# Kernel optimization log

Measured on AMD Instinct MI355X. Metric: run time of the kernel, lower is better.

## Reference

```python
import jax, jax.numpy as jnp
import numpy as np

SIZE = (2, 2)


def setup_inputs() -> dict:
    key = jax.random.key(0)
    k1, k2 = jax.random.split(key)
    B, H, W, C = 32, 64, 64, 128
    out_flat = (H * SIZE[0]) * (W * SIZE[1]) * C  # 2,097,152
    updates = jax.random.normal(k1, (B, H, W, C), dtype=jnp.float32)
    mask = jax.random.randint(k2, (B, H, W, C), 0, out_flat, dtype=jnp.int32)
    return {"updates": updates, "mask": mask}


def reference(updates, mask):
    B, H, W, C = updates.shape
    outH, outW = H * SIZE[0], W * SIZE[1]
    flat = outH * outW * C
    # batch index broadcast to match mask, then flat scatter (tf.scatter_nd sums duplicates)
    b = jnp.broadcast_to(jnp.arange(B, dtype=jnp.int32)[:, None, None, None], mask.shape)
    ret = jnp.zeros((B, flat), dtype=updates.dtype)
    ret = ret.at[b.reshape(-1), mask.reshape(-1)].add(updates.reshape(-1))
    return ret.reshape(B, outH, outW, C)
```

## Files before the change

kernel.cpp:

```cpp
#include <hip/hip_runtime.h>


typedef float f32x4 __attribute__((ext_vector_type(4)));
typedef int i32x4 __attribute__((ext_vector_type(4)));
typedef unsigned u32x4 __attribute__((ext_vector_type(4)));

constexpr int B = 32;
constexpr int IN_PER_B = 1 << 19;
constexpr int OUT_PER_B = 1 << 21;
constexpr int N = B * IN_PER_B;
constexpr int OUT_N = B * OUT_PER_B;

constexpr int BKT_BITS = 13;
constexpr int BKT_SIZE = 1 << BKT_BITS;
constexpr int NBKT = B * (OUT_PER_B >> BKT_BITS);
constexpr int CAP = 3072;
constexpr int CHUNK = 4096;
constexpr int P1_THREADS = 512;
constexpr int P2_THREADS = 512;
constexpr int P1_BLOCKS = N / CHUNK;
constexpr unsigned DUMP_IDX = (unsigned)NBKT * (unsigned)CAP;
constexpr size_t BINS_BYTES = ((size_t)NBKT * CAP + 16) * 4ull;
constexpr size_t CNT_BYTES = (size_t)NBKT * 4ull;
constexpr size_t WS_NEEDED = BINS_BYTES + CNT_BYTES;

__device__ __forceinline__ unsigned pack_val19(float v) {
  unsigned bits = __float_as_uint(v);
  return (bits + 0x1000u) >> 13;
}
__device__ __forceinline__ float unpack_val19(unsigned p) {
  return __uint_as_float(p << 13);
}

__global__ __launch_bounds__(P1_THREADS) void p1_bin(const i32x4* __restrict__ msk,
                                                     const f32x4* __restrict__ upd,
                                                     unsigned* __restrict__ bins,
                                                     int* __restrict__ cnt) {
  __shared__ int hist[256];
  __shared__ int wsum[4];
  __shared__ unsigned adjg[256];
  __shared__ unsigned lsthr[256];
  __shared__ uint2 sdata[CHUNK];

  const int t = threadIdx.x;
  const int blk = blockIdx.x;
  const int b = blk >> 7;
  const long c4 = (long)blk * (CHUNK / 4);

  if (t < 256) hist[t] = 0;

  i32x4 m[2];
  f32x4 u[2];
#pragma unroll
  for (int k = 0; k < 2; k++) {
    m[k] = __builtin_nontemporal_load(&msk[c4 + k * P1_THREADS + t]);
    u[k] = __builtin_nontemporal_load(&upd[c4 + k * P1_THREADS + t]);
  }
  __syncthreads();

  int rank[8];
#pragma unroll
  for (int k = 0; k < 2; k++) {
#pragma unroll
    for (int c = 0; c < 4; c++)
      rank[k * 4 + c] = atomicAdd(&hist[m[k][c] >> BKT_BITS], 1);
  }
  __syncthreads();

  int h = 0, v = 0;
  if (t < 256) {
    h = hist[t];
    v = h;
#pragma unroll
    for (int off = 1; off < 64; off <<= 1) {
      int pv = __shfl_up(v, off);
      if ((t & 63) >= off) v += pv;
    }
    if ((t & 63) == 63) wsum[t >> 6] = v;
  }
  __syncthreads();
  if (t < 256) {
    const int w = t >> 6;
    int pre = 0;
    if (w > 0) pre += wsum[0];
    if (w > 1) pre += wsum[1];
    if (w > 2) pre += wsum[2];
    const int ls = pre + v - h;
    const int gb = (b << 8) + t;
    const int cbase = (h > 0) ? atomicAdd(&cnt[gb], h) : 0;
    adjg[t] = (unsigned)gb * (unsigned)CAP + (unsigned)(cbase - ls);
    int thr = CAP - cbase;
    thr = thr < 0 ? 0 : (thr > 0xFFFF ? 0xFFFF : thr);
    lsthr[t] = (unsigned)ls | ((unsigned)thr << 16);
  }
  __syncthreads();

#pragma unroll
  for (int k = 0; k < 2; k++) {
#pragma unroll
    for (int c = 0; c < 4; c++) {
      const int idx = m[k][c];
      const int bkt = idx >> BKT_BITS;
      const unsigned lt = lsthr[bkt];
      const int r = rank[k * 4 + c];
      const int pos = (int)(lt & 0xFFFFu) + r;
      unsigned g = adjg[bkt] + (unsigned)pos;
      if ((unsigned)r >= (lt >> 16)) g = DUMP_IDX;
      const unsigned pair =
          ((unsigned)(idx & (BKT_SIZE - 1)) << 19) | pack_val19(u[k][c]);
      sdata[pos] = make_uint2(pair, g);
    }
  }
  __syncthreads();

  const uint4* s4 = (const uint4*)sdata;
#pragma unroll
  for (int k = 0; k < CHUNK / 2 / P1_THREADS; k++) {
    uint4 e = s4[k * P1_THREADS + t];
    bins[e.y] = e.x;
    bins[e.w] = e.z;
  }
}

__global__ __launch_bounds__(P2_THREADS) void p2_acc(const unsigned* __restrict__ bins,
                                                     const int* __restrict__ cnt,
                                                     f32x4* __restrict__ out) {
  __shared__ float acc[BKT_SIZE];
  const int t = threadIdx.x;
  const int gb = blockIdx.x;

  int count = cnt[gb];
  if (count > CAP) count = CAP;
  const long base = (long)gb * CAP;
  const u32x4* b4 = (const u32x4*)(bins + base);
  const int nv = count >> 2;

  u32x4 v0 = (u32x4){0, 0, 0, 0}, v1 = v0;
  const bool h0 = t < nv, h1 = t + P2_THREADS < nv;
  if (h0) v0 = __builtin_nontemporal_load(&b4[t]);
  if (h1) v1 = __builtin_nontemporal_load(&b4[t + P2_THREADS]);
  const int rem = count - (nv << 2);
  unsigned tv = 0;
  const bool ht = t < rem;
  if (ht) tv = bins[base + (nv << 2) + t];

  f32x4* a4 = (f32x4*)acc;
#pragma unroll
  for (int k = 0; k < BKT_SIZE / 4 / P2_THREADS; k++)
    a4[k * P2_THREADS + t] = (f32x4){0.f, 0.f, 0.f, 0.f};
  __syncthreads();

  if (h0) {
    atomicAdd(&acc[v0.x >> 19], unpack_val19(v0.x));
    atomicAdd(&acc[v0.y >> 19], unpack_val19(v0.y));
    atomicAdd(&acc[v0.z >> 19], unpack_val19(v0.z));
    atomicAdd(&acc[v0.w >> 19], unpack_val19(v0.w));
  }
  if (h1) {
    atomicAdd(&acc[v1.x >> 19], unpack_val19(v1.x));
    atomicAdd(&acc[v1.y >> 19], unpack_val19(v1.y));
    atomicAdd(&acc[v1.z >> 19], unpack_val19(v1.z));
    atomicAdd(&acc[v1.w >> 19], unpack_val19(v1.w));
  }
  if (ht) atomicAdd(&acc[tv >> 19], unpack_val19(tv));
  __syncthreads();

  const long ob4 = (long)gb * (BKT_SIZE / 4);
#pragma unroll
  for (int k = 0; k < BKT_SIZE / 4 / P2_THREADS; k++) {
    f32x4 o = a4[k * P2_THREADS + t];
    __builtin_nontemporal_store(o, &out[ob4 + k * P2_THREADS + t]);
  }
}

__global__ __launch_bounds__(256) void zero_kernel(float4* __restrict__ out) {
  int i = blockIdx.x * 256 + threadIdx.x;
  out[i] = make_float4(0.f, 0.f, 0.f, 0.f);
}

__global__ __launch_bounds__(256) void scatter_atomic(const float4* __restrict__ upd,
                                                      const int4* __restrict__ msk,
                                                      float* __restrict__ out) {
  int i = blockIdx.x * 256 + threadIdx.x;
  int4 m = msk[i];
  float4 u = upd[i];
  int b = i >> 17;
  float* outb = out + (long)b * OUT_PER_B;
  unsafeAtomicAdd(outb + m.x, u.x);
  unsafeAtomicAdd(outb + m.y, u.y);
  unsafeAtomicAdd(outb + m.z, u.z);
  unsafeAtomicAdd(outb + m.w, u.w);
}

extern "C" void kernel_launch(void* const* d_in, const int* in_sizes, int n_in,
                              void* d_out, int out_size, void* d_ws, size_t ws_size,
                              hipStream_t stream) {
  if (ws_size >= WS_NEEDED) {
    unsigned* bins = (unsigned*)d_ws;
    int* cnt = (int*)((char*)d_ws + BINS_BYTES);
    (void)hipMemsetAsync(cnt, 0, CNT_BYTES, stream);
    p1_bin<<<P1_BLOCKS, P1_THREADS, 0, stream>>>((const i32x4*)d_in[1],
                                                 (const f32x4*)d_in[0], bins, cnt);
    p2_acc<<<NBKT, P2_THREADS, 0, stream>>>(bins, cnt, (f32x4*)d_out);
  } else {
    zero_kernel<<<OUT_N / 4 / 256, 256, 0, stream>>>((float4*)d_out);
    scatter_atomic<<<N / 4 / 256, 256, 0, stream>>>((const float4*)d_in[0],
                                                    (const int4*)d_in[1],
                                                    (float*)d_out);
  }
}
```

Baseline: 421.0 us.

## Pad bucket segments to multiples of four and emit 16-byte vector bin stores

Each bucket's per-chunk segment is padded to a multiple of four with zero entries, so global bin offsets stay 16-byte aligned. The binning kernel then writes whole groups of four packed pairs with one vector store, keeping only one destination index per group in shared memory. This cuts the number of scattered 4-byte global writes and the shared staging footprint. In exchange the padding adds extra work in the accumulation pass, uses more bin capacity, and puts extra zero adds onto accumulator slot 0; the accumulation kernel also drops its tail handling and its nontemporal loads.

```diff
diff --git a/kernel.cpp b/kernel.cpp
--- a/kernel.cpp
+++ b/kernel.cpp
@@ -19,6 +19,7 @@
 constexpr int P1_THREADS = 512;
 constexpr int P2_THREADS = 512;
 constexpr int P1_BLOCKS = N / CHUNK;
+constexpr int SMAX = CHUNK + 256 * 3;
 constexpr unsigned DUMP_IDX = (unsigned)NBKT * (unsigned)CAP;
 constexpr size_t BINS_BYTES = ((size_t)NBKT * CAP + 16) * 4ull;
 constexpr size_t CNT_BYTES = (size_t)NBKT * 4ull;
@@ -38,9 +39,11 @@
                                                      int* __restrict__ cnt) {
   __shared__ int hist[256];
   __shared__ int wsum[4];
+  __shared__ int stot_s;
   __shared__ unsigned adjg[256];
   __shared__ unsigned lsthr[256];
-  __shared__ uint2 sdata[CHUNK];
+  __shared__ alignas(16) unsigned pairs[SMAX];
+  __shared__ unsigned gq[SMAX / 4];
 
   const int t = threadIdx.x;
   const int blk = blockIdx.x;
@@ -67,10 +70,11 @@
   }
   __syncthreads();
 
-  int h = 0, v = 0;
+  int h = 0, hp = 0, v = 0;
   if (t < 256) {
     h = hist[t];
-    v = h;
+    hp = (h + 3) & ~3;
+    v = hp;
 #pragma unroll
     for (int off = 1; off < 64; off <<= 1) {
       int pv = __shfl_up(v, off);
@@ -85,13 +89,15 @@
     if (w > 0) pre += wsum[0];
     if (w > 1) pre += wsum[1];
     if (w > 2) pre += wsum[2];
-    const int ls = pre + v - h;
+    const int ls = pre + v - hp;
     const int gb = (b << 8) + t;
-    const int cbase = (h > 0) ? atomicAdd(&cnt[gb], h) : 0;
+    const int cbase = (hp > 0) ? atomicAdd(&cnt[gb], hp) : 0;
     adjg[t] = (unsigned)gb * (unsigned)CAP + (unsigned)(cbase - ls);
     int thr = CAP - cbase;
-    thr = thr < 0 ? 0 : (thr > 0xFFFF ? 0xFFFF : thr);
+    thr = thr < 0 ? 0 : thr;
     lsthr[t] = (unsigned)ls | ((unsigned)thr << 16);
+    if (t == 255) stot_s = pre + v;
+    for (int p = h; p < hp; ++p) pairs[ls + p] = 0;
   }
   __syncthreads();
 
@@ -104,21 +110,23 @@
       const unsigned lt = lsthr[bkt];
       const int r = rank[k * 4 + c];
       const int pos = (int)(lt & 0xFFFFu) + r;
-      unsigned g = adjg[bkt] + (unsigned)pos;
-      if ((unsigned)r >= (lt >> 16)) g = DUMP_IDX;
-      const unsigned pair =
+      pairs[pos] =
           ((unsigned)(idx & (BKT_SIZE - 1)) << 19) | pack_val19(u[k][c]);
-      sdata[pos] = make_uint2(pair, g);
+      if ((pos & 3) == 0) {
+        unsigned g = adjg[bkt] + (unsigned)pos;
+        if ((unsigned)r >= (lt >> 16)) g = DUMP_IDX;
+        gq[pos >> 2] = g;
+      }
     }
   }
   __syncthreads();
 
-  const uint4* s4 = (const uint4*)sdata;
-#pragma unroll
-  for (int k = 0; k < CHUNK / 2 / P1_THREADS; k++) {
-    uint4 e = s4[k * P1_THREADS + t];
-    bins[e.y] = e.x;
-    bins[e.w] = e.z;
+  const int ng = stot_s >> 2;
+  const u32x4* p4 = (const u32x4*)pairs;
+  for (int j = t; j < ng; j += P1_THREADS) {
+    u32x4 e = p4[j];
+    unsigned g = gq[j];
+    *(u32x4*)(bins + g) = e;
   }
 }
 
@@ -137,12 +145,8 @@
 
   u32x4 v0 = (u32x4){0, 0, 0, 0}, v1 = v0;
   const bool h0 = t < nv, h1 = t + P2_THREADS < nv;
-  if (h0) v0 = __builtin_nontemporal_load(&b4[t]);
-  if (h1) v1 = __builtin_nontemporal_load(&b4[t + P2_THREADS]);
-  const int rem = count - (nv << 2);
-  unsigned tv = 0;
-  const bool ht = t < rem;
-  if (ht) tv = bins[base + (nv << 2) + t];
+  if (h0) v0 = b4[t];
+  if (h1) v1 = b4[t + P2_THREADS];
 
   f32x4* a4 = (f32x4*)acc;
 #pragma unroll
@@ -162,7 +166,6 @@
     atomicAdd(&acc[v1.z >> 19], unpack_val19(v1.z));
     atomicAdd(&acc[v1.w >> 19], unpack_val19(v1.w));
   }
-  if (ht) atomicAdd(&acc[tv >> 19], unpack_val19(tv));
   __syncthreads();
 
   const long ob4 = (long)gb * (BKT_SIZE / 4);
```

New measurement: 430.2 us. +2.2%, slower.
